# Optimization experiments

Measured on AMD Instinct MI355X. Metric: run time of the kernel, lower is better.

## Reference

```python
import jax, jax.numpy as jnp
import numpy as np
import math

D = 768; H = 8; HD = D // H; T = 1024; V = 32000; M = 10
BLOCK = 128          # flex-attention block size (sliding_window_num_blocks granularity)
TAU = 1.0            # gumbel_temp
MAXC = 10            # max middle-block visits == scan length
EPS = 1e-6
IFP = 0.95           # initial_forward_prob

def rms(x):
    return x * jax.lax.rsqrt(jnp.mean(x * x, axis=-1, keepdims=True) + EPS)

def make_rope(t):
    # Rotary.__init__: dim//4 real inv freqs + dim//4 zeros -> cos/sin of shape [t, HD//2]
    inv = (1.0 / 1024) ** jnp.linspace(0.0, 1.0, HD // 4)
    inv = jnp.concatenate([inv, jnp.zeros(HD // 4)])
    th = jnp.arange(t, dtype=jnp.float32)[:, None] * inv[None, :]
    return jnp.cos(th), jnp.sin(th)

def rope(x, cos, sin):
    # x: [1,T,H,HD]
    c = cos[None, :, None, :]; s = sin[None, :, None, :]
    x1, x2 = jnp.split(x, 2, axis=-1)
    return jnp.concatenate([x1 * c + x2 * s, -x1 * s + x2 * c], axis=-1)

def attn(x, ve, wq, wk, wv, wo, lam, cos, sin, mask):
    q = (x @ wq.T).reshape(1, T, H, HD)
    k = (x @ wk.T).reshape(1, T, H, HD)
    v = (x @ wv.T).reshape(1, T, H, HD)
    if ve is not None:
        v = lam[0] * v + lam[1] * ve.reshape(1, T, H, HD)
    else:
        v = lam[0] * v
    q = rope(rms(q), cos, sin); k = rope(rms(k), cos, sin)
    sc = jnp.einsum('bthd,bshd->bhts', q, k) * (1.0 / math.sqrt(HD))
    sc = jnp.where(mask, sc, -1e30)
    y = jnp.einsum('bhts,bshd->bthd', jax.nn.softmax(sc, axis=-1), v).reshape(1, T, D)
    return y @ wo.T

def mlp(x, fc, pr):
    return jnp.square(jax.nn.relu(x @ fc.T)) @ pr.T

def fwd(tokens, embed_w, ve_w, lm_head_w,
        in_wq, in_wk, in_wv, in_wo, in_attn_lam, in_fc, in_pr, in_lam,
        mid_wq, mid_wk, mid_wv, mid_wo, mid_attn_lam, mid_fc, mid_pr, router_w, router_b,
        out_wq, out_wk, out_wv, out_wo, out_attn_lam, out_fc, out_pr, out_lam,
        gumbel_u, window_blocks, max_block_count):
    cos, sin = make_rope(T)
    qi = jnp.arange(T)
    mask = ((qi[:, None] >= qi[None, :]) &
            ((qi[:, None] // BLOCK - qi[None, :] // BLOCK) < window_blocks))[None, None]
    x = rms(embed_w[tokens][None])     # norm(embed(inputs))
    x0 = x
    ve = ve_w[tokens][None]            # X=1 value embedding, reused for output block
    # ---- input FixedBlock ----
    h = in_lam[0] * x + in_lam[1] * x0
    h = h + attn(rms(h), ve, in_wq, in_wk, in_wv, in_wo, in_attn_lam, cos, sin, mask)
    h = h + mlp(rms(h), in_fc, in_pr)
    # ---- middle routing loop (fixed-length scan, masked once exited) ----
    g = -jnp.log(-jnp.log(gumbel_u + 1e-10) + 1e-10)  # [MAXC, M+1] gumbel noise
    mbc = jnp.float32(max_block_count)
    def step(carry, gi):
        x, cur, done, cnt = carry
        y = x + attn(rms(x), None, mid_wq[cur], mid_wk[cur], mid_wv[cur], mid_wo[cur],
                     mid_attn_lam[cur], cos, sin, mask)
        y = y + mlp(rms(y), mid_fc[cur], mid_pr[cur])
        feat = jnp.concatenate([y.mean(axis=1), jnp.stack([cnt, mbc])[None]], axis=-1)  # [1, D+2]
        logits = feat @ router_w[cur].T + router_b[cur]                                  # [1, M+1]
        route = jax.nn.softmax((logits + gi[None]) / TAU, axis=-1)
        nxt = jnp.argmax(route[0]).astype(jnp.int32)
        new_cnt = cnt + 1.0
        exit_now = (nxt == M) | (new_cnt >= mbc)
        x = jnp.where(done, x, y)
        cnt = jnp.where(done, cnt, new_cnt)
        new_done = done | exit_now
        cur = jnp.where(new_done, cur, nxt)
        return (x, cur, new_done, cnt), None
    init = (h, jnp.int32(0), jnp.bool_(False), jnp.float32(0.0))
    (x, _, _, _), _ = jax.lax.scan(step, init, g)
    # ---- output FixedBlock ----
    y = out_lam[0] * x + out_lam[1] * x0
    y = y + attn(rms(y), ve, out_wq, out_wk, out_wv, out_wo, out_attn_lam, cos, sin, mask)
    y = y + mlp(rms(y), out_fc, out_pr)
    logits = rms(y) @ lm_head_w.T
    return 30.0 * jnp.tanh(logits / 30.0)

def setup_inputs() -> dict:
    key = jax.random.key(0)
    ks = iter(jax.random.split(key, 64))
    def w(*s, std=0.02):
        return (std * jax.random.normal(next(ks), s)).astype(jnp.float32)
    rb = np.full((M, M + 1), math.log((1.0 - IFP) / M), dtype=np.float32)
    for i in range(M):
        rb[i, min(i + 1, M)] = math.log(IFP)
    inp = {
        'tokens': jax.random.randint(next(ks), (T,), 0, V, dtype=jnp.int32),
        'embed_w': w(V, D), 've_w': w(V, D), 'lm_head_w': w(V, D),
        'in_wq': w(D, D), 'in_wk': w(D, D), 'in_wv': w(D, D), 'in_wo': w(D, D),
        'in_attn_lam': jnp.array([0.5, 0.5], jnp.float32),
        'in_fc': w(4 * D, D), 'in_pr': w(D, 4 * D),
        'in_lam': jnp.array([1.0, 0.0], jnp.float32),
        'mid_wq': w(M, D, D), 'mid_wk': w(M, D, D), 'mid_wv': w(M, D, D), 'mid_wo': w(M, D, D),
        'mid_attn_lam': jnp.tile(jnp.array([0.5, 0.5], jnp.float32), (M, 1)),
        'mid_fc': w(M, 4 * D, D), 'mid_pr': w(M, D, 4 * D),
        'router_w': w(M, M + 1, D + 2, std=0.001),
        'router_b': jnp.asarray(rb),
        'out_wq': w(D, D), 'out_wk': w(D, D), 'out_wv': w(D, D), 'out_wo': w(D, D),
        'out_attn_lam': jnp.array([0.5, 0.5], jnp.float32),
        'out_fc': w(4 * D, D), 'out_pr': w(D, 4 * D),
        'out_lam': jnp.array([1.0, 0.0], jnp.float32),
        'gumbel_u': jax.random.uniform(next(ks), (MAXC, M + 1), dtype=jnp.float32),
        'window_blocks': 4,
        'max_block_count': MAXC,
    }
    return inp

def reference(tokens, embed_w, ve_w, lm_head_w,
              in_wq, in_wk, in_wv, in_wo, in_attn_lam, in_fc, in_pr, in_lam,
              mid_wq, mid_wk, mid_wv, mid_wo, mid_attn_lam, mid_fc, mid_pr, router_w, router_b,
              out_wq, out_wk, out_wv, out_wo, out_attn_lam, out_fc, out_pr, out_lam,
              gumbel_u, window_blocks, max_block_count):
    return fwd(tokens, embed_w, ve_w, lm_head_w,
               in_wq, in_wk, in_wv, in_wo, in_attn_lam, in_fc, in_pr, in_lam,
               mid_wq, mid_wk, mid_wv, mid_wo, mid_attn_lam, mid_fc, mid_pr, router_w, router_b,
               out_wq, out_wk, out_wv, out_wo, out_attn_lam, out_fc, out_pr, out_lam,
               gumbel_u, window_blocks, max_block_count)
```

## Files before the change

### kernel.cpp

```cpp
#include <hip/hip_runtime.h>
#include <hip/hip_bf16.h>

namespace {

constexpr int cT   = 1024;
constexpr int cD   = 768;
constexpr int cH   = 8;
constexpr int cHD  = 96;
constexpr int cM   = 10;
constexpr int cDff = 3072;
constexpr int cV   = 32000;
constexpr int cTD  = cT * cD;
constexpr float cEps = 1e-6f;

constexpr long oWQ = 0;
constexpr long oWK = 589824;
constexpr long oWV = 2L * 589824;
constexpr long oWO = 3L * 589824;
constexpr long oFC = 4L * 589824;
constexpr long oPR = 4L * 589824 + 2359296;
constexpr long cWTOT = 4L * 589824 + 2L * 2359296;
constexpr int cConvBlocks = (int)(cWTOT / 8 / 256);

typedef __attribute__((ext_vector_type(8))) short short8;
typedef __attribute__((ext_vector_type(4))) float f32x4;

__device__ inline short bf16r(float f) {
  union { float f; unsigned u; } x{f};
  unsigned r = (x.u + 0x7FFF + ((x.u >> 16) & 1)) >> 16;
  return (short)r;
}

__device__ inline float bf2f(short s) {
  union { unsigned u; float f; } x;
  x.u = ((unsigned)(unsigned short)s) << 16;
  return x.f;
}


__global__ void init_state_k(int* cur, int* done, float* cnt, float* feat) {
  if (threadIdx.x == 0) { *cur = 0; *done = 0; *cnt = 0.0f; }
  for (int d = threadIdx.x; d < cD; d += 256) feat[d] = 0.f;
}

__global__ void rope_pre_k(float* __restrict__ cosb, float* __restrict__ sinb) {
  int idx = blockIdx.x * blockDim.x + threadIdx.x;
  if (idx >= cT * 48) return;
  int t = idx / 48, j = idx % 48;
  float th = 0.0f;
  if (j < 24) th = (float)t * powf(1.0f / 1024.0f, (float)j / 23.0f);
  cosb[idx] = cosf(th);
  sinb[idx] = sinf(th);
}

__global__ __launch_bounds__(256) void embed_rms_k(const int* __restrict__ tok,
    const float* __restrict__ ew, const float* __restrict__ vw,
    float* __restrict__ x0, float* __restrict__ ve) {
  int t = blockIdx.x;
  int tk = tok[t];
  const float* er = ew + (size_t)tk * cD;
  const float* vr = vw + (size_t)tk * cD;
  __shared__ float red[256];
  float s = 0.f;
  for (int d = threadIdx.x; d < cD; d += 256) { float e = er[d]; s += e * e; }
  red[threadIdx.x] = s; __syncthreads();
  for (int st = 128; st; st >>= 1) { if (threadIdx.x < st) red[threadIdx.x] += red[threadIdx.x + st]; __syncthreads(); }
  float sc = rsqrtf(red[0] / cD + cEps);
  for (int d = threadIdx.x; d < cD; d += 256) {
    x0[(size_t)t * cD + d] = er[d] * sc;
    ve[(size_t)t * cD + d] = vr[d];
  }
}

__global__ __launch_bounds__(256) void rms_rows_bf(const float* __restrict__ in,
    short* __restrict__ out, const int* done) {
  if (done && *done) return;
  int t = blockIdx.x;
  const float* r = in + (size_t)t * cD;
  __shared__ float red[256];
  float s = 0.f;
  for (int d = threadIdx.x; d < cD; d += 256) { float v = r[d]; s += v * v; }
  red[threadIdx.x] = s; __syncthreads();
  for (int st = 128; st; st >>= 1) { if (threadIdx.x < st) red[threadIdx.x] += red[threadIdx.x + st]; __syncthreads(); }
  float sc = rsqrtf(red[0] / cD + cEps);
  short* o = out + (size_t)t * cD;
  for (int d = threadIdx.x; d < cD; d += 256) o[d] = bf16r(r[d] * sc);
}

__global__ void axpy_lam_k(const float* __restrict__ lam, const float* __restrict__ a,
                           const float* __restrict__ b, float* __restrict__ o, int n) {
  int i = blockIdx.x * 256 + threadIdx.x;
  if (i < n) o[i] = lam[0] * a[i] + lam[1] * b[i];
}


__global__ __launch_bounds__(256) void layer_pre_k(const float* __restrict__ s0,
    const float* __restrict__ s1, const float* __restrict__ s2, const float* __restrict__ s3,
    const float* __restrict__ s4, const float* __restrict__ s5, short* __restrict__ dst,
    const int* __restrict__ cur, const int* __restrict__ done,
    const float* __restrict__ xin, short* __restrict__ xnbf, float* __restrict__ rsum) {
  if (done && *done) return;
  const int b = blockIdx.x;
  if (b < cConvBlocks) {
    long e = ((long)b * 256 + threadIdx.x) * 8;
    long cu = cur ? (long)(*cur) : 0L;
    const float* src;
    if (e < oWK)      src = s0 + cu * 589824  + e;
    else if (e < oWV) src = s1 + cu * 589824  + (e - oWK);
    else if (e < oWO) src = s2 + cu * 589824  + (e - oWV);
    else if (e < oFC) src = s3 + cu * 589824  + (e - oWO);
    else if (e < oPR) src = s4 + cu * 2359296 + (e - oFC);
    else              src = s5 + cu * 2359296 + (e - oPR);
    float4 a0 = *(const float4*)src;
    float4 a1 = *(const float4*)(src + 4);
    short8 sv;
    sv[0]=bf16r(a0.x); sv[1]=bf16r(a0.y); sv[2]=bf16r(a0.z); sv[3]=bf16r(a0.w);
    sv[4]=bf16r(a1.x); sv[5]=bf16r(a1.y); sv[6]=bf16r(a1.z); sv[7]=bf16r(a1.w);
    *(short8*)(dst + e) = sv;
  } else {
    const int t = b - cConvBlocks;
    const float* r = xin + (size_t)t * cD;
    __shared__ float red[256];
    float s = 0.f;
    for (int d = threadIdx.x; d < cD; d += 256) { float v = r[d]; s += v * v; }
    red[threadIdx.x] = s; __syncthreads();
    for (int st = 128; st; st >>= 1) { if (threadIdx.x < st) red[threadIdx.x] += red[threadIdx.x + st]; __syncthreads(); }
    float sc = rsqrtf(red[0] / cD + cEps);
    short* o = xnbf + (size_t)t * cD;
    for (int d = threadIdx.x; d < cD; d += 256) o[d] = bf16r(r[d] * sc);
    if (threadIdx.x == 0) rsum[t] = 0.f;
  }
}

__global__ __launch_bounds__(256) void conv1_k(const float* __restrict__ src,
    short* __restrict__ dst, long nchunk) {
  long i = (long)blockIdx.x * 256 + threadIdx.x;
  if (i >= nchunk) return;
  long e = i * 8;
  float4 a0 = *(const float4*)(src + e);
  float4 a1 = *(const float4*)(src + e + 4);
  short8 sv;
  sv[0]=bf16r(a0.x); sv[1]=bf16r(a0.y); sv[2]=bf16r(a0.z); sv[3]=bf16r(a0.w);
  sv[4]=bf16r(a1.x); sv[5]=bf16r(a1.y); sv[6]=bf16r(a1.z); sv[7]=bf16r(a1.w);
  *(short8*)(dst + e) = sv;
}


__global__ __launch_bounds__(256) void qkv_k(const short* __restrict__ A,
    const short* __restrict__ Wb,
    short* __restrict__ qo, short* __restrict__ ko, short* __restrict__ vo,
    const int* __restrict__ done, const float* __restrict__ lamb,
    const int* __restrict__ cur, const float* __restrict__ vep,
    const float* __restrict__ cosb, const float* __restrict__ sinb) {
  if (done && *done) return;
  const int z = blockIdx.z;
  const short* W = Wb + (long)z * 589824L;
  const int h  = blockIdx.x;
  const int bm = blockIdx.y * 64;
  __shared__ short As[2][64][40];
  __shared__ short Bs[2][96][40];
  const int tid = threadIdx.x;
  const int w = tid >> 6, lane = tid & 63;
  const int fr = lane & 15, fg = lane >> 4;
  const int ar = tid >> 2, ac2 = (tid & 3) << 3;
  const int br1 = (256 + tid) >> 2, bc1 = ((256 + tid) & 3) << 3;

  short8 aN, bN0, bN1;
  aN  = *(const short8*)(A + (size_t)(bm + ar) * cD + ac2);
  bN0 = *(const short8*)(W + (size_t)(h * cHD + ar) * cD + ac2);
  if (tid < 128) bN1 = *(const short8*)(W + (size_t)(h * cHD + br1) * cD + bc1);
  *(short8*)&As[0][ar][ac2] = aN;
  *(short8*)&Bs[0][ar][ac2] = bN0;
  if (tid < 128) *(short8*)&Bs[0][br1][bc1] = bN1;
  __syncthreads();

  f32x4 acc[6] = {};
  int cb = 0;
  for (int kt = 0; kt < cD; kt += 32) {
    const int ktn = kt + 32;
    const bool hn = ktn < cD;
    if (hn) {
      aN  = *(const short8*)(A + (size_t)(bm + ar) * cD + ktn + ac2);
      bN0 = *(const short8*)(W + (size_t)(h * cHD + ar) * cD + ktn + ac2);
      if (tid < 128) bN1 = *(const short8*)(W + (size_t)(h * cHD + br1) * cD + ktn + bc1);
    }
    short8 af = *(const short8*)&As[cb][w * 16 + fr][fg * 8];
#pragma unroll
    for (int n = 0; n < 6; ++n) {
      short8 bf = *(const short8*)&Bs[cb][n * 16 + fr][fg * 8];
      acc[n] = __builtin_amdgcn_mfma_f32_16x16x32_bf16(af, bf, acc[n], 0, 0, 0);
    }
    if (hn) {
      *(short8*)&As[cb ^ 1][ar][ac2] = aN;
      *(short8*)&Bs[cb ^ 1][ar][ac2] = bN0;
      if (tid < 128) *(short8*)&Bs[cb ^ 1][br1][bc1] = bN1;
    }
    __syncthreads();
    cb ^= 1;
  }

  const int t0 = bm + w * 16 + fg * 4;
  if (z < 2) {
    float scl[4];
#pragma unroll
    for (int r = 0; r < 4; ++r) {
      float s = 0.f;
#pragma unroll
      for (int n = 0; n < 6; ++n) s += acc[n][r] * acc[n][r];
#pragma unroll
      for (int mm = 1; mm < 16; mm <<= 1) s += __shfl_xor(s, mm, 64);
      scl[r] = rsqrtf(s * (1.0f / 96.0f) + cEps);
    }
    short* C = (z == 0 ? qo : ko);
#pragma unroll
    for (int r = 0; r < 4; ++r) {
      int t = t0 + r;
      short* orow = C + (size_t)t * cD + h * cHD;
#pragma unroll
      for (int n = 0; n < 3; ++n) {
        int j = n * 16 + fr;
        float c = cosb[t * 48 + j], sn = sinb[t * 48 + j];
        float x1 = acc[n][r] * scl[r], x2 = acc[n + 3][r] * scl[r];
        orow[j]      = bf16r(x1 * c + x2 * sn);
        orow[j + 48] = bf16r(-x1 * sn + x2 * c);
      }
    }
  } else {
    int cu = cur ? *cur : 0;
    float l0 = lamb[2 * cu], l1 = lamb[2 * cu + 1];
#pragma unroll
    for (int r = 0; r < 4; ++r) {
      int t = t0 + r;
#pragma unroll
      for (int n = 0; n < 6; ++n) {
        float val = l0 * acc[n][r];
        if (vep) val += l1 * vep[(size_t)t * cD + h * cHD + n * 16 + fr];
        vo[(size_t)t * cD + h * cHD + n * 16 + fr] = bf16r(val);
      }
    }
  }
}


__global__ __launch_bounds__(256) void attn_f(const short* __restrict__ q,
    const short* __restrict__ k, const short* __restrict__ v, short* __restrict__ o,
    const int* __restrict__ wbp, const int* done) {
  if (done && *done) return;
  const int qb = blockIdx.x;
  const int h  = blockIdx.y;
  const int q0 = qb * 64;
  const int qb128 = q0 >> 7;
  const int wb = *wbp;
  int kb_lo = qb128 - wb + 1; if (kb_lo < 0) kb_lo = 0;

  __shared__ short Ksh[128][136];
  __shared__ short Vt[96][136];

  const int tid  = threadIdx.x;
  const int w    = tid >> 6;
  const int lane = tid & 63;
  const int fr   = lane & 15;
  const int fg   = lane >> 4;

  short8 qf[3];
  {
    const short* qrow = q + (size_t)(q0 + w * 16 + fr) * cD + h * cHD;
#pragma unroll
    for (int ks = 0; ks < 3; ++ks) qf[ks] = *(const short8*)(qrow + ks * 32 + fg * 8);
  }

  f32x4 accO[6] = {};
  float mrun[4], lrun[4];
#pragma unroll
  for (int r = 0; r < 4; ++r) { mrun[r] = -1e30f; lrun[r] = 0.f; }

  for (int kb = kb_lo; kb <= qb128; ++kb) {
    __syncthreads();
    const int key0 = kb * 128;
#pragma unroll
    for (int c = 0; c < 6; ++c) {
      int idx = c * 256 + tid;
      int row = idx / 12, colc = (idx % 12) * 8;
      *(short8*)&Ksh[row][colc] =
          *(const short8*)(k + (size_t)(key0 + row) * cD + h * cHD + colc);
      short8 vv = *(const short8*)(v + (size_t)(key0 + row) * cD + h * cHD + colc);
#pragma unroll
      for (int i = 0; i < 8; ++i) Vt[colc + i][row] = vv[i];
    }
    __syncthreads();

    f32x4 s[8];
#pragma unroll
    for (int n = 0; n < 8; ++n) s[n] = (f32x4){0.f, 0.f, 0.f, 0.f};
#pragma unroll
    for (int ks = 0; ks < 3; ++ks) {
#pragma unroll
      for (int n = 0; n < 8; ++n) {
        short8 kf = *(const short8*)&Ksh[n * 16 + fr][ks * 32 + fg * 8];
        s[n] = __builtin_amdgcn_mfma_f32_16x16x32_bf16(qf[ks], kf, s[n], 0, 0, 0);
      }
    }

    float pmax[4] = {-1e30f, -1e30f, -1e30f, -1e30f};
#pragma unroll
    for (int n = 0; n < 8; ++n)
#pragma unroll
      for (int r = 0; r < 4; ++r) {
        float val = s[n][r] * 0.10206207261596577f;
        int key  = key0 + n * 16 + fr;
        int qrow = q0 + w * 16 + fg * 4 + r;
        if (key > qrow) val = -1e30f;
        s[n][r] = val;
        pmax[r] = fmaxf(pmax[r], val);
      }
#pragma unroll
    for (int mm = 1; mm < 16; mm <<= 1)
#pragma unroll
      for (int r = 0; r < 4; ++r) pmax[r] = fmaxf(pmax[r], __shfl_xor(pmax[r], mm, 64));
    float alpha[4], psum[4];
#pragma unroll
    for (int r = 0; r < 4; ++r) {
      float mn = fmaxf(mrun[r], pmax[r]);
      alpha[r] = __expf(mrun[r] - mn);
      mrun[r] = mn;
      psum[r] = 0.f;
    }
#pragma unroll
    for (int n = 0; n < 8; ++n)
#pragma unroll
      for (int r = 0; r < 4; ++r) {
        float p = __expf(s[n][r] - mrun[r]);
        s[n][r] = p;
        psum[r] += p;
      }
#pragma unroll
    for (int mm = 1; mm < 16; mm <<= 1)
#pragma unroll
      for (int r = 0; r < 4; ++r) psum[r] += __shfl_xor(psum[r], mm, 64);
#pragma unroll
    for (int r = 0; r < 4; ++r) lrun[r] = lrun[r] * alpha[r] + psum[r];
#pragma unroll
    for (int n = 0; n < 6; ++n) {
      f32x4 t = accO[n];
#pragma unroll
      for (int r = 0; r < 4; ++r) t[r] *= alpha[r];
      accO[n] = t;
    }

    __syncthreads();
#pragma unroll
    for (int n = 0; n < 8; ++n)
#pragma unroll
      for (int r = 0; r < 4; ++r)
        Ksh[w * 16 + fg * 4 + r][n * 16 + fr] = bf16r(s[n][r]);
    __syncthreads();

#pragma unroll
    for (int ks = 0; ks < 4; ++ks) {
      short8 pf = *(const short8*)&Ksh[w * 16 + fr][ks * 32 + fg * 8];
#pragma unroll
      for (int n = 0; n < 6; ++n) {
        short8 vf = *(const short8*)&Vt[n * 16 + fr][ks * 32 + fg * 8];
        accO[n] = __builtin_amdgcn_mfma_f32_16x16x32_bf16(pf, vf, accO[n], 0, 0, 0);
      }
    }
  }

#pragma unroll
  for (int r = 0; r < 4; ++r) {
    float inv = 1.0f / lrun[r];
    int t = q0 + w * 16 + fg * 4 + r;
#pragma unroll
    for (int n = 0; n < 6; ++n)
      o[(size_t)t * cD + h * cHD + n * 16 + fr] = bf16r(accO[n][r] * inv);
  }
}


template <int EPI, typename OT>
__global__ __launch_bounds__(256) void gemm64_k(const short* __restrict__ A,
    const short* __restrict__ W, OT* __restrict__ C, const int* __restrict__ done,
    const float* __restrict__ res, float* __restrict__ rsum, int ld, int kn, int N) {
  if (done && *done) return;
  const int bm = blockIdx.y * 64;
  const int bn = blockIdx.x * 64;
  const int k0 = blockIdx.z * kn;
  __shared__ short As[2][64][40];
  __shared__ short Bs[2][64][40];
  const int tid = threadIdx.x;
  const int wid = tid >> 6, lane = tid & 63;
  const int wr = wid >> 1, wc = wid & 1;
  const int fr = lane & 15, fg = lane >> 4;
  const int ar = tid >> 2, ac = (tid & 3) << 3;

  short8 aN = *(const short8*)(A + (size_t)(bm + ar) * ld + k0 + ac);
  short8 bN = *(const short8*)(W + (size_t)(bn + ar) * ld + k0 + ac);
  *(short8*)&As[0][ar][ac] = aN;
  *(short8*)&Bs[0][ar][ac] = bN;
  __syncthreads();

  f32x4 acc[2][2] = {};
  int cb = 0;
  for (int kt = 0; kt < kn; kt += 32) {
    const int ktn = kt + 32;
    const bool hn = ktn < kn;
    if (hn) {
      aN = *(const short8*)(A + (size_t)(bm + ar) * ld + k0 + ktn + ac);
      bN = *(const short8*)(W + (size_t)(bn + ar) * ld + k0 + ktn + ac);
    }
    short8 af[2], bfv[2];
#pragma unroll
    for (int m = 0; m < 2; ++m) af[m] = *(const short8*)&As[cb][wr * 32 + m * 16 + fr][fg * 8];
#pragma unroll
    for (int n = 0; n < 2; ++n) bfv[n] = *(const short8*)&Bs[cb][wc * 32 + n * 16 + fr][fg * 8];
#pragma unroll
    for (int m = 0; m < 2; ++m)
#pragma unroll
      for (int n = 0; n < 2; ++n)
        acc[m][n] = __builtin_amdgcn_mfma_f32_16x16x32_bf16(af[m], bfv[n], acc[m][n], 0, 0, 0);
    if (hn) {
      *(short8*)&As[cb ^ 1][ar][ac] = aN;
      *(short8*)&Bs[cb ^ 1][ar][ac] = bN;
    }
    __syncthreads();
    cb ^= 1;
  }
#pragma unroll
  for (int m = 0; m < 2; ++m)
#pragma unroll
    for (int r = 0; r < 4; ++r) {
      const int row = bm + wr * 32 + m * 16 + fg * 4 + r;
      float p = 0.f;
#pragma unroll
      for (int n = 0; n < 2; ++n) {
        const int col = bn + wc * 32 + n * 16 + fr;
        float val = acc[m][n][r];
        if constexpr (EPI == 1) {
          val += res[(size_t)row * N + col];
          C[(size_t)row * N + col] = val;
          p += val * val;
        } else {
          C[(size_t)blockIdx.z * cTD + (size_t)row * N + col] = (OT)bf16r(val);
        }
      }
      if constexpr (EPI == 1) {
#pragma unroll
        for (int mm = 1; mm < 16; mm <<= 1) p += __shfl_xor(p, mm, 64);
        if (fr == 0) atomicAdd(&rsum[row], p);
      }
    }
}


__global__ __launch_bounds__(256) void mgemm_fc_k(const float* __restrict__ Ay,
    const float* __restrict__ rsum, const short* __restrict__ W, short* __restrict__ C,
    const int* __restrict__ done, int K, int N) {
  if (done && *done) return;
  const int bm = blockIdx.y * 64;
  const int bn = blockIdx.x * 128;
  __shared__ short As[2][64][40];
  __shared__ short Bs[2][128][40];
  const int tid = threadIdx.x;
  const int wid = tid >> 6, lane = tid & 63;
  const int wr = wid >> 1, wc = wid & 1;
  const int fr = lane & 15, fg = lane >> 4;
  const int ar = tid >> 2, ac = (tid & 3) << 3;
  const int br1 = (256 + tid) >> 2, bc1 = ((256 + tid) & 3) << 3;

  const float ascl = rsqrtf(rsum[bm + ar] * (1.0f / cD) + cEps);
  const float* arow = Ay + (size_t)(bm + ar) * K;

  auto loadA = [&](int kt) -> short8 {
    float4 a0 = *(const float4*)(arow + kt + ac);
    float4 a1 = *(const float4*)(arow + kt + ac + 4);
    short8 sv;
    sv[0]=bf16r(a0.x*ascl); sv[1]=bf16r(a0.y*ascl); sv[2]=bf16r(a0.z*ascl); sv[3]=bf16r(a0.w*ascl);
    sv[4]=bf16r(a1.x*ascl); sv[5]=bf16r(a1.y*ascl); sv[6]=bf16r(a1.z*ascl); sv[7]=bf16r(a1.w*ascl);
    return sv;
  };

  short8 aN, bN0, bN1;
  aN  = loadA(0);
  bN0 = *(const short8*)(W + (size_t)(bn + ar) * K + ac);
  bN1 = *(const short8*)(W + (size_t)(bn + br1) * K + bc1);
  *(short8*)&As[0][ar][ac] = aN;
  *(short8*)&Bs[0][ar][ac] = bN0;
  *(short8*)&Bs[0][br1][bc1] = bN1;
  __syncthreads();

  f32x4 acc[2][4] = {};
  int cb = 0;
  for (int kt = 0; kt < K; kt += 32) {
    const int ktn = kt + 32;
    const bool hn = ktn < K;
    if (hn) {
      aN  = loadA(ktn);
      bN0 = *(const short8*)(W + (size_t)(bn + ar) * K + ktn + ac);
      bN1 = *(const short8*)(W + (size_t)(bn + br1) * K + ktn + bc1);
    }
    short8 af[2], bfv[4];
#pragma unroll
    for (int m = 0; m < 2; ++m) af[m] = *(const short8*)&As[cb][wr * 32 + m * 16 + fr][fg * 8];
#pragma unroll
    for (int n = 0; n < 4; ++n) bfv[n] = *(const short8*)&Bs[cb][wc * 64 + n * 16 + fr][fg * 8];
#pragma unroll
    for (int m = 0; m < 2; ++m)
#pragma unroll
      for (int n = 0; n < 4; ++n)
        acc[m][n] = __builtin_amdgcn_mfma_f32_16x16x32_bf16(af[m], bfv[n], acc[m][n], 0, 0, 0);
    if (hn) {
      *(short8*)&As[cb ^ 1][ar][ac] = aN;
      *(short8*)&Bs[cb ^ 1][ar][ac] = bN0;
      *(short8*)&Bs[cb ^ 1][br1][bc1] = bN1;
    }
    __syncthreads();
    cb ^= 1;
  }
#pragma unroll
  for (int m = 0; m < 2; ++m)
#pragma unroll
    for (int n = 0; n < 4; ++n)
#pragma unroll
      for (int r = 0; r < 4; ++r) {
        int row = bm + wr * 32 + m * 16 + fg * 4 + r;
        int col = bn + wc * 64 + n * 16 + fr;
        float val = acc[m][n][r];
        val = fmaxf(val, 0.f); val = val * val;
        C[(size_t)row * N + col] = bf16r(val);
      }
}


__global__ __launch_bounds__(256) void reduce_k(const short* __restrict__ pb,
    float* __restrict__ y, float* __restrict__ x, float* __restrict__ feat,
    const int* done) {
  if (done && *done) return;
  __shared__ float red[256];
  const int d = blockIdx.x * 32 + (threadIdx.x & 31);
  const int tc = threadIdx.x >> 5;
  const int t0 = blockIdx.y * 128 + tc * 16;
  float s = 0.f;
  for (int t = t0; t < t0 + 16; ++t) {
    size_t i = (size_t)t * cD + d;
    float v = y[i];
#pragma unroll
    for (int z = 0; z < 4; ++z) v += bf2f(pb[(size_t)z * cTD + i]);
    y[i] = v;
    if (x) x[i] = v;
    s += v;
  }
  if (feat) {
    red[threadIdx.x] = s; __syncthreads();
    if (threadIdx.x < 32) {
      float tot = 0.f;
#pragma unroll
      for (int c = 0; c < 8; ++c) tot += red[c * 32 + threadIdx.x];
      atomicAdd(&feat[d], tot * (1.0f / cT));
    }
  }
}


__global__ void router_step_k(float* __restrict__ feat, const float* __restrict__ rw,
    const float* __restrict__ rb, const float* __restrict__ gu, int iter,
    const int* __restrict__ mbcp, int* cur, int* done, float* cnt) {
  if (*done) return;
  __shared__ float lg[cM + 1];
  const int tid = threadIdx.x;
  const int c = *cur;
  const float mbc = (float)(*mbcp);
  const float cn = *cnt;
  for (int j = 0; j < cM + 1; ++j) {
    const float* w = rw + ((size_t)c * (cM + 1) + j) * (cD + 2);
    float s = 0.f;
    for (int d = tid; d < cD; d += 64) s += feat[d] * w[d];
#pragma unroll
    for (int mm = 32; mm; mm >>= 1) s += __shfl_xor(s, mm, 64);
    if (tid == 0) {
      s += cn * w[cD] + mbc * w[cD + 1] + rb[c * (cM + 1) + j];
      float u = gu[iter * (cM + 1) + j];
      float inner = -logf(u + 1e-10f) + 1e-10f;
      lg[j] = s - logf(inner);
    }
  }
  __syncthreads();
  for (int d = tid; d < cD; d += 64) feat[d] = 0.f;
  if (tid == 0) {
    int nxt = 0; float best = lg[0];
    for (int j = 1; j < cM + 1; ++j) if (lg[j] > best) { best = lg[j]; nxt = j; }
    float nc = cn + 1.0f;
    int ex = (nxt == cM) || (nc >= mbc);
    *cnt = nc;
    if (ex) *done = 1; else *cur = nxt;
  }
}


__global__ __launch_bounds__(512) void gemm_lm_k(const short* __restrict__ A,
    const short* __restrict__ W, float* __restrict__ C) {
  const int nwg = (cV / 128) * (cT / 256);
  const int cpx = nwg / 8;
  const int swz = (blockIdx.x % 8) * cpx + blockIdx.x / 8;
  const int bm = (swz % 4) * 256;
  const int bn = (swz / 4) * 128;
  __shared__ short As[2][256][40];
  __shared__ short Bs[2][128][40];
  const int tid = threadIdx.x;
  const int wid = tid >> 6, lane = tid & 63;
  const int wr = wid >> 1, wc = wid & 1;
  const int fr = lane & 15, fg = lane >> 4;
  const int ar0 = tid >> 2, ac0 = (tid & 3) << 3;
  const int ar1 = (512 + tid) >> 2, ac1 = ((512 + tid) & 3) << 3;

  short8 aN0, aN1, bN;
  aN0 = *(const short8*)(A + (size_t)(bm + ar0) * cD + ac0);
  aN1 = *(const short8*)(A + (size_t)(bm + ar1) * cD + ac1);
  bN  = *(const short8*)(W + (size_t)(bn + ar0) * cD + ac0);
  *(short8*)&As[0][ar0][ac0] = aN0;
  *(short8*)&As[0][ar1][ac1] = aN1;
  *(short8*)&Bs[0][ar0][ac0] = bN;
  __syncthreads();

  f32x4 acc[4][4] = {};
  int cb = 0;
  for (int kt = 0; kt < cD; kt += 32) {
    const int ktn = kt + 32;
    const bool hn = ktn < cD;
    if (hn) {
      aN0 = *(const short8*)(A + (size_t)(bm + ar0) * cD + ktn + ac0);
      aN1 = *(const short8*)(A + (size_t)(bm + ar1) * cD + ktn + ac1);
      bN  = *(const short8*)(W + (size_t)(bn + ar0) * cD + ktn + ac0);
    }
    short8 af[4], bfv[4];
#pragma unroll
    for (int m = 0; m < 4; ++m) af[m] = *(const short8*)&As[cb][wr * 64 + m * 16 + fr][fg * 8];
#pragma unroll
    for (int n = 0; n < 4; ++n) bfv[n] = *(const short8*)&Bs[cb][wc * 64 + n * 16 + fr][fg * 8];
#pragma unroll
    for (int m = 0; m < 4; ++m)
#pragma unroll
      for (int n = 0; n < 4; ++n)
        acc[m][n] = __builtin_amdgcn_mfma_f32_16x16x32_bf16(af[m], bfv[n], acc[m][n], 0, 0, 0);
    if (hn) {
      *(short8*)&As[cb ^ 1][ar0][ac0] = aN0;
      *(short8*)&As[cb ^ 1][ar1][ac1] = aN1;
      *(short8*)&Bs[cb ^ 1][ar0][ac0] = bN;
    }
    __syncthreads();
    cb ^= 1;
  }
#pragma unroll
  for (int m = 0; m < 4; ++m)
#pragma unroll
    for (int n = 0; n < 4; ++n)
#pragma unroll
      for (int r = 0; r < 4; ++r) {
        int row = bm + wr * 64 + m * 16 + fg * 4 + r;
        int col = bn + wc * 64 + n * 16 + fr;
        C[(size_t)row * cV + col] = 30.f * tanhf(acc[m][n][r] * (1.f / 30.f));
      }
}

}


extern "C" void kernel_launch(void* const* d_in, const int* in_sizes, int n_in,
                              void* d_out, int out_size, void* d_ws, size_t ws_size,
                              hipStream_t stream) {
  const int*   tokens    = (const int*)d_in[0];
  const float* embed_w   = (const float*)d_in[1];
  const float* ve_w      = (const float*)d_in[2];
  const float* lm_head_w = (const float*)d_in[3];
  const float* in_wq  = (const float*)d_in[4];
  const float* in_wk  = (const float*)d_in[5];
  const float* in_wv  = (const float*)d_in[6];
  const float* in_wo  = (const float*)d_in[7];
  const float* in_al  = (const float*)d_in[8];
  const float* in_fc  = (const float*)d_in[9];
  const float* in_pr  = (const float*)d_in[10];
  const float* in_lam = (const float*)d_in[11];
  const float* mid_wq = (const float*)d_in[12];
  const float* mid_wk = (const float*)d_in[13];
  const float* mid_wv = (const float*)d_in[14];
  const float* mid_wo = (const float*)d_in[15];
  const float* mid_al = (const float*)d_in[16];
  const float* mid_fc = (const float*)d_in[17];
  const float* mid_pr = (const float*)d_in[18];
  const float* router_w = (const float*)d_in[19];
  const float* router_b = (const float*)d_in[20];
  const float* out_wq = (const float*)d_in[21];
  const float* out_wk = (const float*)d_in[22];
  const float* out_wv = (const float*)d_in[23];
  const float* out_wo = (const float*)d_in[24];
  const float* out_al = (const float*)d_in[25];
  const float* out_fc = (const float*)d_in[26];
  const float* out_pr = (const float*)d_in[27];
  const float* out_lam = (const float*)d_in[28];
  const float* gumbel_u = (const float*)d_in[29];
  const int*   wbp  = (const int*)d_in[30];
  const int*   mbcp = (const int*)d_in[31];
  float* outp = (float*)d_out;

  float* ws = (float*)d_ws;
  float* xb   = ws;
  float* x0b  = xb  + cTD;
  float* veb  = x0b + cTD;
  float* yb   = veb + cTD;
  float* cosb = yb  + cTD;
  float* sinb = cosb + cT * 48;
  float* rsum = sinb + cT * 48;
  float* feat = rsum + 1024;
  int*   curp  = (int*)(feat + 784);
  int*   donep = curp + 1;
  float* cntp  = (float*)(curp + 2);
  short* xnbf  = (short*)(feat + 784 + 8);
  short* aobf  = xnbf + cTD;
  short* qbf   = aobf + cTD;
  short* kbf   = qbf  + cTD;
  short* vbf   = kbf  + cTD;
  short* pbuf  = aobf;
  short* hidbf = vbf  + cTD;
  short* wbf   = hidbf + (size_t)cT * cDff;

  const dim3 gPre(cConvBlocks + cT, 1, 1);
  const dim3 gQKV(cH, cT / 64, 3);
  const dim3 gWO(cD / 64, cT / 64, 1);
  const dim3 gPR(cD / 64, cT / 64, 4);
  const dim3 gFF(cDff / 128, cT / 64, 1);
  const dim3 gLM(1000, 1, 1);
  const dim3 gAttn(cT / 64, cH, 1);
  const dim3 gRed(cD / 32, 8, 1);
  const long lmChunks = (long)cV * cD / 8;
  const int gConvLM = (int)(lmChunks / 256);

  auto layer = [&](const float* wq, const float* wk, const float* wv, const float* wo,
                   const float* alam, const float* fc, const float* pr,
                   const int* cur, const int* done,
                   float* xin, float* yout, const float* vept,
                   float* xcom, float* featp) {
    layer_pre_k<<<gPre, 256, 0, stream>>>(wq, wk, wv, wo, fc, pr, wbf, cur, done,
                                          xin, xnbf, rsum);
    qkv_k<<<gQKV, 256, 0, stream>>>(xnbf, wbf, qbf, kbf, vbf, done, alam, cur, vept,
                                    cosb, sinb);
    attn_f<<<gAttn, 256, 0, stream>>>(qbf, kbf, vbf, aobf, wbp, done);
    gemm64_k<1, float><<<gWO, 256, 0, stream>>>(aobf, wbf + oWO, yout, done, xin, rsum,
                                                cD, cD, cD);
    mgemm_fc_k<<<gFF, 256, 0, stream>>>(yout, rsum, wbf + oFC, hidbf, done, cD, cDff);
    gemm64_k<4, short><<<gPR, 256, 0, stream>>>(hidbf, wbf + oPR, pbuf, done, nullptr,
                                                nullptr, cDff, cDff / 4, cD);
    reduce_k<<<gRed, 256, 0, stream>>>(pbuf, yout, xcom, featp, done);
  };

  init_state_k<<<1, 256, 0, stream>>>(curp, donep, cntp, feat);
  rope_pre_k<<<(cT * 48 + 255) / 256, 256, 0, stream>>>(cosb, sinb);
  embed_rms_k<<<cT, 256, 0, stream>>>(tokens, embed_w, ve_w, x0b, veb);

  axpy_lam_k<<<cTD / 256, 256, 0, stream>>>(in_lam, x0b, x0b, xb, cTD);
  layer(in_wq, in_wk, in_wv, in_wo, in_al, in_fc, in_pr, nullptr, nullptr,
        xb, xb, veb, nullptr, nullptr);

  for (int it = 0; it < cM; ++it) {
    layer(mid_wq, mid_wk, mid_wv, mid_wo, mid_al, mid_fc, mid_pr,
          curp, donep, xb, yb, nullptr, xb, feat);
    router_step_k<<<1, 64, 0, stream>>>(feat, router_w, router_b, gumbel_u, it, mbcp,
                                        curp, donep, cntp);
  }

  axpy_lam_k<<<cTD / 256, 256, 0, stream>>>(out_lam, xb, x0b, xb, cTD);
  layer(out_wq, out_wk, out_wv, out_wo, out_al, out_fc, out_pr, nullptr, nullptr,
        xb, xb, veb, nullptr, nullptr);

  conv1_k<<<gConvLM, 256, 0, stream>>>(lm_head_w, wbf, lmChunks);
  rms_rows_bf<<<cT, 256, 0, stream>>>(xb, xnbf, nullptr);
  gemm_lm_k<<<gLM, 512, 0, stream>>>(xnbf, wbf, outp);
}
```

Before: 2.131 ms.

## Fuse fp32-to-bf16 weight conversion into GEMM tile loads

Drops the separate per-layer and lm_head weight conversion passes that wrote bf16 copies of the weights. Each GEMM kernel (qkv, wo, fc, proj, lm_head) now reads fp32 weights directly and rounds them to bf16 while staging tiles into shared memory, with the middle-block weight slice chosen on device from the current index. This saves a full weight write and re-read per layer, but doubles the weight bytes fetched inside the GEMMs and repeats the conversion in every tile that re-reads the same weights (e.g. across the 1000 lm_head workgroups).

```diff
diff --git a/kernel.cpp b/kernel.cpp
--- a/kernel.cpp
+++ b/kernel.cpp
@@ -13,15 +13,6 @@
 constexpr int cTD  = cT * cD;
 constexpr float cEps = 1e-6f;
 
-constexpr long oWQ = 0;
-constexpr long oWK = 589824;
-constexpr long oWV = 2L * 589824;
-constexpr long oWO = 3L * 589824;
-constexpr long oFC = 4L * 589824;
-constexpr long oPR = 4L * 589824 + 2359296;
-constexpr long cWTOT = 4L * 589824 + 2L * 2359296;
-constexpr int cConvBlocks = (int)(cWTOT / 8 / 256);
-
 typedef __attribute__((ext_vector_type(8))) short short8;
 typedef __attribute__((ext_vector_type(4))) float f32x4;
 
@@ -35,6 +26,15 @@
   union { unsigned u; float f; } x;
   x.u = ((unsigned)(unsigned short)s) << 16;
   return x.f;
+}
+
+__device__ inline short8 ld8cvt(const float* __restrict__ p) {
+  float4 a0 = *(const float4*)p;
+  float4 a1 = *(const float4*)(p + 4);
+  short8 sv;
+  sv[0]=bf16r(a0.x); sv[1]=bf16r(a0.y); sv[2]=bf16r(a0.z); sv[3]=bf16r(a0.w);
+  sv[4]=bf16r(a1.x); sv[5]=bf16r(a1.y); sv[6]=bf16r(a1.z); sv[7]=bf16r(a1.w);
+  return sv;
 }
 
 
@@ -87,6 +87,22 @@
   for (int d = threadIdx.x; d < cD; d += 256) o[d] = bf16r(r[d] * sc);
 }
 
+__global__ __launch_bounds__(256) void rms_pre_k(const float* __restrict__ in,
+    short* __restrict__ out, float* __restrict__ rsum, const int* done) {
+  if (done && *done) return;
+  int t = blockIdx.x;
+  const float* r = in + (size_t)t * cD;
+  __shared__ float red[256];
+  float s = 0.f;
+  for (int d = threadIdx.x; d < cD; d += 256) { float v = r[d]; s += v * v; }
+  red[threadIdx.x] = s; __syncthreads();
+  for (int st = 128; st; st >>= 1) { if (threadIdx.x < st) red[threadIdx.x] += red[threadIdx.x + st]; __syncthreads(); }
+  float sc = rsqrtf(red[0] / cD + cEps);
+  short* o = out + (size_t)t * cD;
+  for (int d = threadIdx.x; d < cD; d += 256) o[d] = bf16r(r[d] * sc);
+  if (threadIdx.x == 0) rsum[t] = 0.f;
+}
+
 __global__ void axpy_lam_k(const float* __restrict__ lam, const float* __restrict__ a,
                            const float* __restrict__ b, float* __restrict__ o, int n) {
   int i = blockIdx.x * 256 + threadIdx.x;
@@ -94,67 +110,16 @@
 }
 
 
-__global__ __launch_bounds__(256) void layer_pre_k(const float* __restrict__ s0,
-    const float* __restrict__ s1, const float* __restrict__ s2, const float* __restrict__ s3,
-    const float* __restrict__ s4, const float* __restrict__ s5, short* __restrict__ dst,
-    const int* __restrict__ cur, const int* __restrict__ done,
-    const float* __restrict__ xin, short* __restrict__ xnbf, float* __restrict__ rsum) {
-  if (done && *done) return;
-  const int b = blockIdx.x;
-  if (b < cConvBlocks) {
-    long e = ((long)b * 256 + threadIdx.x) * 8;
-    long cu = cur ? (long)(*cur) : 0L;
-    const float* src;
-    if (e < oWK)      src = s0 + cu * 589824  + e;
-    else if (e < oWV) src = s1 + cu * 589824  + (e - oWK);
-    else if (e < oWO) src = s2 + cu * 589824  + (e - oWV);
-    else if (e < oFC) src = s3 + cu * 589824  + (e - oWO);
-    else if (e < oPR) src = s4 + cu * 2359296 + (e - oFC);
-    else              src = s5 + cu * 2359296 + (e - oPR);
-    float4 a0 = *(const float4*)src;
-    float4 a1 = *(const float4*)(src + 4);
-    short8 sv;
-    sv[0]=bf16r(a0.x); sv[1]=bf16r(a0.y); sv[2]=bf16r(a0.z); sv[3]=bf16r(a0.w);
-    sv[4]=bf16r(a1.x); sv[5]=bf16r(a1.y); sv[6]=bf16r(a1.z); sv[7]=bf16r(a1.w);
-    *(short8*)(dst + e) = sv;
-  } else {
-    const int t = b - cConvBlocks;
-    const float* r = xin + (size_t)t * cD;
-    __shared__ float red[256];
-    float s = 0.f;
-    for (int d = threadIdx.x; d < cD; d += 256) { float v = r[d]; s += v * v; }
-    red[threadIdx.x] = s; __syncthreads();
-    for (int st = 128; st; st >>= 1) { if (threadIdx.x < st) red[threadIdx.x] += red[threadIdx.x + st]; __syncthreads(); }
-    float sc = rsqrtf(red[0] / cD + cEps);
-    short* o = xnbf + (size_t)t * cD;
-    for (int d = threadIdx.x; d < cD; d += 256) o[d] = bf16r(r[d] * sc);
-    if (threadIdx.x == 0) rsum[t] = 0.f;
-  }
-}
-
-__global__ __launch_bounds__(256) void conv1_k(const float* __restrict__ src,
-    short* __restrict__ dst, long nchunk) {
-  long i = (long)blockIdx.x * 256 + threadIdx.x;
-  if (i >= nchunk) return;
-  long e = i * 8;
-  float4 a0 = *(const float4*)(src + e);
-  float4 a1 = *(const float4*)(src + e + 4);
-  short8 sv;
-  sv[0]=bf16r(a0.x); sv[1]=bf16r(a0.y); sv[2]=bf16r(a0.z); sv[3]=bf16r(a0.w);
-  sv[4]=bf16r(a1.x); sv[5]=bf16r(a1.y); sv[6]=bf16r(a1.z); sv[7]=bf16r(a1.w);
-  *(short8*)(dst + e) = sv;
-}
-
-
 __global__ __launch_bounds__(256) void qkv_k(const short* __restrict__ A,
-    const short* __restrict__ Wb,
+    const float* __restrict__ Wq, const float* __restrict__ Wk, const float* __restrict__ Wv,
     short* __restrict__ qo, short* __restrict__ ko, short* __restrict__ vo,
     const int* __restrict__ done, const float* __restrict__ lamb,
     const int* __restrict__ cur, const float* __restrict__ vep,
     const float* __restrict__ cosb, const float* __restrict__ sinb) {
   if (done && *done) return;
   const int z = blockIdx.z;
-  const short* W = Wb + (long)z * 589824L;
+  const long cu = cur ? (long)(*cur) : 0L;
+  const float* W = (z == 0 ? Wq : z == 1 ? Wk : Wv) + cu * 589824L;
   const int h  = blockIdx.x;
   const int bm = blockIdx.y * 64;
   __shared__ short As[2][64][40];
@@ -167,8 +132,8 @@
 
   short8 aN, bN0, bN1;
   aN  = *(const short8*)(A + (size_t)(bm + ar) * cD + ac2);
-  bN0 = *(const short8*)(W + (size_t)(h * cHD + ar) * cD + ac2);
-  if (tid < 128) bN1 = *(const short8*)(W + (size_t)(h * cHD + br1) * cD + bc1);
+  bN0 = ld8cvt(W + (size_t)(h * cHD + ar) * cD + ac2);
+  if (tid < 128) bN1 = ld8cvt(W + (size_t)(h * cHD + br1) * cD + bc1);
   *(short8*)&As[0][ar][ac2] = aN;
   *(short8*)&Bs[0][ar][ac2] = bN0;
   if (tid < 128) *(short8*)&Bs[0][br1][bc1] = bN1;
@@ -181,8 +146,8 @@
     const bool hn = ktn < cD;
     if (hn) {
       aN  = *(const short8*)(A + (size_t)(bm + ar) * cD + ktn + ac2);
-      bN0 = *(const short8*)(W + (size_t)(h * cHD + ar) * cD + ktn + ac2);
-      if (tid < 128) bN1 = *(const short8*)(W + (size_t)(h * cHD + br1) * cD + ktn + bc1);
+      bN0 = ld8cvt(W + (size_t)(h * cHD + ar) * cD + ktn + ac2);
+      if (tid < 128) bN1 = ld8cvt(W + (size_t)(h * cHD + br1) * cD + ktn + bc1);
     }
     short8 af = *(const short8*)&As[cb][w * 16 + fr][fg * 8];
 #pragma unroll
@@ -226,8 +191,8 @@
       }
     }
   } else {
-    int cu = cur ? *cur : 0;
-    float l0 = lamb[2 * cu], l1 = lamb[2 * cu + 1];
+    int cu2 = cur ? *cur : 0;
+    float l0 = lamb[2 * cu2], l1 = lamb[2 * cu2 + 1];
 #pragma unroll
     for (int r = 0; r < 4; ++r) {
       int t = t0 + r;
@@ -379,9 +344,11 @@
 
 template <int EPI, typename OT>
 __global__ __launch_bounds__(256) void gemm64_k(const short* __restrict__ A,
-    const short* __restrict__ W, OT* __restrict__ C, const int* __restrict__ done,
+    const float* __restrict__ Wf, const int* __restrict__ wcur, long sstr,
+    OT* __restrict__ C, const int* __restrict__ done,
     const float* __restrict__ res, float* __restrict__ rsum, int ld, int kn, int N) {
   if (done && *done) return;
+  const float* W = Wf + (wcur ? (long)(*wcur) * sstr : 0L);
   const int bm = blockIdx.y * 64;
   const int bn = blockIdx.x * 64;
   const int k0 = blockIdx.z * kn;
@@ -394,7 +361,7 @@
   const int ar = tid >> 2, ac = (tid & 3) << 3;
 
   short8 aN = *(const short8*)(A + (size_t)(bm + ar) * ld + k0 + ac);
-  short8 bN = *(const short8*)(W + (size_t)(bn + ar) * ld + k0 + ac);
+  short8 bN = ld8cvt(W + (size_t)(bn + ar) * ld + k0 + ac);
   *(short8*)&As[0][ar][ac] = aN;
   *(short8*)&Bs[0][ar][ac] = bN;
   __syncthreads();
@@ -406,7 +373,7 @@
     const bool hn = ktn < kn;
     if (hn) {
       aN = *(const short8*)(A + (size_t)(bm + ar) * ld + k0 + ktn + ac);
-      bN = *(const short8*)(W + (size_t)(bn + ar) * ld + k0 + ktn + ac);
+      bN = ld8cvt(W + (size_t)(bn + ar) * ld + k0 + ktn + ac);
     }
     short8 af[2], bfv[2];
 #pragma unroll
@@ -453,9 +420,11 @@
 
 
 __global__ __launch_bounds__(256) void mgemm_fc_k(const float* __restrict__ Ay,
-    const float* __restrict__ rsum, const short* __restrict__ W, short* __restrict__ C,
+    const float* __restrict__ rsum, const float* __restrict__ Wf,
+    const int* __restrict__ wcur, long sstr, short* __restrict__ C,
     const int* __restrict__ done, int K, int N) {
   if (done && *done) return;
+  const float* W = Wf + (wcur ? (long)(*wcur) * sstr : 0L);
   const int bm = blockIdx.y * 64;
   const int bn = blockIdx.x * 128;
   __shared__ short As[2][64][40];
@@ -481,8 +450,8 @@
 
   short8 aN, bN0, bN1;
   aN  = loadA(0);
-  bN0 = *(const short8*)(W + (size_t)(bn + ar) * K + ac);
-  bN1 = *(const short8*)(W + (size_t)(bn + br1) * K + bc1);
+  bN0 = ld8cvt(W + (size_t)(bn + ar) * K + ac);
+  bN1 = ld8cvt(W + (size_t)(bn + br1) * K + bc1);
   *(short8*)&As[0][ar][ac] = aN;
   *(short8*)&Bs[0][ar][ac] = bN0;
   *(short8*)&Bs[0][br1][bc1] = bN1;
@@ -495,8 +464,8 @@
     const bool hn = ktn < K;
     if (hn) {
       aN  = loadA(ktn);
-      bN0 = *(const short8*)(W + (size_t)(bn + ar) * K + ktn + ac);
-      bN1 = *(const short8*)(W + (size_t)(bn + br1) * K + ktn + bc1);
+      bN0 = ld8cvt(W + (size_t)(bn + ar) * K + ktn + ac);
+      bN1 = ld8cvt(W + (size_t)(bn + br1) * K + ktn + bc1);
     }
     short8 af[2], bfv[4];
 #pragma unroll
@@ -597,7 +566,7 @@
 
 
 __global__ __launch_bounds__(512) void gemm_lm_k(const short* __restrict__ A,
-    const short* __restrict__ W, float* __restrict__ C) {
+    const float* __restrict__ W, float* __restrict__ C) {
   const int nwg = (cV / 128) * (cT / 256);
   const int cpx = nwg / 8;
   const int swz = (blockIdx.x % 8) * cpx + blockIdx.x / 8;
@@ -615,7 +584,7 @@
   short8 aN0, aN1, bN;
   aN0 = *(const short8*)(A + (size_t)(bm + ar0) * cD + ac0);
   aN1 = *(const short8*)(A + (size_t)(bm + ar1) * cD + ac1);
-  bN  = *(const short8*)(W + (size_t)(bn + ar0) * cD + ac0);
+  bN  = ld8cvt(W + (size_t)(bn + ar0) * cD + ac0);
   *(short8*)&As[0][ar0][ac0] = aN0;
   *(short8*)&As[0][ar1][ac1] = aN1;
   *(short8*)&Bs[0][ar0][ac0] = bN;
@@ -629,7 +598,7 @@
     if (hn) {
       aN0 = *(const short8*)(A + (size_t)(bm + ar0) * cD + ktn + ac0);
       aN1 = *(const short8*)(A + (size_t)(bm + ar1) * cD + ktn + ac1);
-      bN  = *(const short8*)(W + (size_t)(bn + ar0) * cD + ktn + ac0);
+      bN  = ld8cvt(W + (size_t)(bn + ar0) * cD + ktn + ac0);
     }
     short8 af[4], bfv[4];
 #pragma unroll
@@ -720,9 +689,7 @@
   short* vbf   = kbf  + cTD;
   short* pbuf  = aobf;
   short* hidbf = vbf  + cTD;
-  short* wbf   = hidbf + (size_t)cT * cDff;
-
-  const dim3 gPre(cConvBlocks + cT, 1, 1);
+
   const dim3 gQKV(cH, cT / 64, 3);
   const dim3 gWO(cD / 64, cT / 64, 1);
   const dim3 gPR(cD / 64, cT / 64, 4);
@@ -730,23 +697,20 @@
   const dim3 gLM(1000, 1, 1);
   const dim3 gAttn(cT / 64, cH, 1);
   const dim3 gRed(cD / 32, 8, 1);
-  const long lmChunks = (long)cV * cD / 8;
-  const int gConvLM = (int)(lmChunks / 256);
 
   auto layer = [&](const float* wq, const float* wk, const float* wv, const float* wo,
                    const float* alam, const float* fc, const float* pr,
-                   const int* cur, const int* done,
+                   long sQ, long sF, const int* cur, const int* done,
                    float* xin, float* yout, const float* vept,
                    float* xcom, float* featp) {
-    layer_pre_k<<<gPre, 256, 0, stream>>>(wq, wk, wv, wo, fc, pr, wbf, cur, done,
-                                          xin, xnbf, rsum);
-    qkv_k<<<gQKV, 256, 0, stream>>>(xnbf, wbf, qbf, kbf, vbf, done, alam, cur, vept,
-                                    cosb, sinb);
+    rms_pre_k<<<cT, 256, 0, stream>>>(xin, xnbf, rsum, done);
+    qkv_k<<<gQKV, 256, 0, stream>>>(xnbf, wq, wk, wv, qbf, kbf, vbf, done, alam,
+                                    cur, vept, cosb, sinb);
     attn_f<<<gAttn, 256, 0, stream>>>(qbf, kbf, vbf, aobf, wbp, done);
-    gemm64_k<1, float><<<gWO, 256, 0, stream>>>(aobf, wbf + oWO, yout, done, xin, rsum,
-                                                cD, cD, cD);
-    mgemm_fc_k<<<gFF, 256, 0, stream>>>(yout, rsum, wbf + oFC, hidbf, done, cD, cDff);
-    gemm64_k<4, short><<<gPR, 256, 0, stream>>>(hidbf, wbf + oPR, pbuf, done, nullptr,
+    gemm64_k<1, float><<<gWO, 256, 0, stream>>>(aobf, wo, cur, sQ, yout, done, xin,
+                                                rsum, cD, cD, cD);
+    mgemm_fc_k<<<gFF, 256, 0, stream>>>(yout, rsum, fc, cur, sF, hidbf, done, cD, cDff);
+    gemm64_k<4, short><<<gPR, 256, 0, stream>>>(hidbf, pr, cur, sF, pbuf, done, nullptr,
                                                 nullptr, cDff, cDff / 4, cD);
     reduce_k<<<gRed, 256, 0, stream>>>(pbuf, yout, xcom, featp, done);
   };
@@ -756,21 +720,20 @@
   embed_rms_k<<<cT, 256, 0, stream>>>(tokens, embed_w, ve_w, x0b, veb);
 
   axpy_lam_k<<<cTD / 256, 256, 0, stream>>>(in_lam, x0b, x0b, xb, cTD);
-  layer(in_wq, in_wk, in_wv, in_wo, in_al, in_fc, in_pr, nullptr, nullptr,
+  layer(in_wq, in_wk, in_wv, in_wo, in_al, in_fc, in_pr, 0L, 0L, nullptr, nullptr,
         xb, xb, veb, nullptr, nullptr);
 
   for (int it = 0; it < cM; ++it) {
     layer(mid_wq, mid_wk, mid_wv, mid_wo, mid_al, mid_fc, mid_pr,
-          curp, donep, xb, yb, nullptr, xb, feat);
+          589824L, 2359296L, curp, donep, xb, yb, nullptr, xb, feat);
     router_step_k<<<1, 64, 0, stream>>>(feat, router_w, router_b, gumbel_u, it, mbcp,
                                         curp, donep, cntp);
   }
 
   axpy_lam_k<<<cTD / 256, 256, 0, stream>>>(out_lam, xb, x0b, xb, cTD);
-  layer(out_wq, out_wk, out_wv, out_wo, out_al, out_fc, out_pr, nullptr, nullptr,
+  layer(out_wq, out_wk, out_wv, out_wo, out_al, out_fc, out_pr, 0L, 0L, nullptr, nullptr,
         xb, xb, veb, nullptr, nullptr);
 
-  conv1_k<<<gConvLM, 256, 0, stream>>>(lm_head_w, wbf, lmChunks);
   rms_rows_bf<<<cT, 256, 0, stream>>>(xb, xnbf, nullptr);
-  gemm_lm_k<<<gLM, 512, 0, stream>>>(xnbf, wbf, outp);
-}
+  gemm_lm_k<<<gLM, 512, 0, stream>>>(xnbf, lm_head_w, outp);
+}
```

New measurement: 2.639 ms. +23.8%, slower.
